# Kernel tuning notes

Hardware: AMD Instinct MI355X
Metric: run time of the kernel (lower is better)

Reference implementation:

```python
import jax, jax.numpy as jnp
import numpy as np
from jax import lax

D_MODEL = 64      # feature_dim
D_STATE = 16      # state_dim
D_CONV = 4        # conv_dim
EXPAND = 2
D_INNER = EXPAND * D_MODEL          # 128
DT_RANK = (D_MODEL + 15) // 16      # ceil(d_model/16) = 4, mamba default
IN_DIM = 64
LN_EPS = 1e-3                        # keras LayerNormalization default epsilon


def setup_inputs() -> dict:
    key = jax.random.key(0)
    ks = jax.random.split(key, 12)
    B, L = 16, 8192
    s = 0.02
    x = jax.random.normal(ks[0], (B, L, IN_DIM), jnp.float32)
    W_in = jax.random.normal(ks[1], (IN_DIM, D_MODEL), jnp.float32) * s
    b_in = jnp.zeros((D_MODEL,), jnp.float32)
    in_proj_w = jax.random.normal(ks[2], (D_MODEL, 2 * D_INNER), jnp.float32) * s
    conv_w = jax.random.normal(ks[3], (D_INNER, D_CONV), jnp.float32) * 0.1
    conv_b = jnp.zeros((D_INNER,), jnp.float32)
    x_proj_w = jax.random.normal(ks[4], (D_INNER, DT_RANK + 2 * D_STATE), jnp.float32) * s
    dt_proj_w = jax.random.normal(ks[5], (DT_RANK, D_INNER), jnp.float32) * (DT_RANK ** -0.5)
    # dt bias init so softplus(dt) lands roughly in [dt_min, dt_max]
    dt = jnp.exp(jax.random.uniform(ks[6], (D_INNER,)) * (np.log(0.1) - np.log(0.001)) + np.log(0.001))
    dt_proj_b = dt + jnp.log(-jnp.expm1(-dt))  # inverse softplus
    A_log = jnp.log(jnp.broadcast_to(jnp.arange(1, D_STATE + 1, dtype=jnp.float32), (D_INNER, D_STATE)))
    D_skip = jnp.ones((D_INNER,), jnp.float32)
    out_proj_w = jax.random.normal(ks[7], (D_INNER, D_MODEL), jnp.float32) * s
    ln_gamma = jnp.ones((D_MODEL,), jnp.float32)
    ln_beta = jnp.zeros((D_MODEL,), jnp.float32)
    return {"x": x, "W_in": W_in, "b_in": b_in, "in_proj_w": in_proj_w,
            "conv_w": conv_w, "conv_b": conv_b, "x_proj_w": x_proj_w,
            "dt_proj_w": dt_proj_w, "dt_proj_b": dt_proj_b, "A_log": A_log,
            "D_skip": D_skip, "out_proj_w": out_proj_w,
            "ln_gamma": ln_gamma, "ln_beta": ln_beta}


def reference(x, W_in, b_in, in_proj_w, conv_w, conv_b, x_proj_w,
              dt_proj_w, dt_proj_b, A_log, D_skip, out_proj_w, ln_gamma, ln_beta):
    B, L, _ = x.shape
    # Conv1D kernel_size=1 input projection
    xin = x @ W_in + b_in                          # [B,L,D_MODEL]
    # --- Mamba ---
    xz = xin @ in_proj_w                           # [B,L,2*D_INNER]
    xc, z = xz[..., :D_INNER], xz[..., D_INNER:]
    # causal depthwise conv (groups=d_inner, padding=d_conv-1, crop to L)
    xp = jnp.pad(xc, ((0, 0), (D_CONV - 1, 0), (0, 0)))
    xconv = conv_b
    for k in range(D_CONV):
        xconv = xconv + xp[:, k:k + L, :] * conv_w[:, k]
    u = jax.nn.silu(xconv)                         # [B,L,D_INNER]
    dbc = u @ x_proj_w                             # [B,L,DT_RANK+2*D_STATE]
    dt = jax.nn.softplus(dbc[..., :DT_RANK] @ dt_proj_w + dt_proj_b)   # [B,L,D_INNER]
    Bm = dbc[..., DT_RANK:DT_RANK + D_STATE]       # [B,L,D_STATE]
    Cm = dbc[..., DT_RANK + D_STATE:]              # [B,L,D_STATE]
    A = -jnp.exp(A_log)                            # [D_INNER,D_STATE]

    def step(h, xs):
        dt_t, b_t, c_t, u_t = xs                   # [B,Di],[B,Ds],[B,Ds],[B,Di]
        dA = jnp.exp(dt_t[:, :, None] * A)         # [B,Di,Ds]
        h = dA * h + (dt_t * u_t)[:, :, None] * b_t[:, None, :]
        y = jnp.einsum('bds,bs->bd', h, c_t)
        return h, y

    xs = (jnp.swapaxes(dt, 0, 1), jnp.swapaxes(Bm, 0, 1),
          jnp.swapaxes(Cm, 0, 1), jnp.swapaxes(u, 0, 1))
    h0 = jnp.zeros((B, D_INNER, D_STATE), x.dtype)
    _, ys = lax.scan(step, h0, xs)                 # ys: [L,B,D_INNER]
    y = jnp.swapaxes(ys, 0, 1) + u * D_skip
    y = y * jax.nn.silu(z)
    h_out = y @ out_proj_w                         # [B,L,D_MODEL]
    # residual + LayerNorm
    res = h_out + xin
    mu = jnp.mean(res, axis=-1, keepdims=True)
    var = jnp.mean(jnp.square(res - mu), axis=-1, keepdims=True)
    return ln_gamma * (res - mu) * lax.rsqrt(var + LN_EPS) + ln_beta
```

## Files before the change

### kernel.cpp

```cpp
#include <hip/hip_runtime.h>
#include <hip/hip_bf16.h>

#define B_SZ   16
#define L_SZ   8192
#define DM     64
#define DI     128
#define NCH    128
#define CLEN   64
#define CH     64
#define RT     80
#define PA     72
#define PU     136
#define PC     132
#define LN_EPS 1e-3f

typedef float  f4 __attribute__((ext_vector_type(4)));
typedef short  s8 __attribute__((ext_vector_type(8)));
typedef unsigned short u16;
typedef unsigned int   u32;
#define MFMA16 __builtin_amdgcn_mfma_f32_16x16x32_bf16

__device__ __forceinline__ u16 f2bfu(float f) {
    u32 u = __float_as_uint(f);
    return (u16)((u + 0x7FFFu + ((u >> 16) & 1u)) >> 16);
}
__device__ __forceinline__ u32 pk2bf(float a, float b) {
    return (u32)f2bfu(a) | ((u32)f2bfu(b) << 16);
}
__device__ __forceinline__ float bflo(u32 u) { return __uint_as_float(u << 16); }
__device__ __forceinline__ float bfhi(u32 u) { return __uint_as_float(u & 0xFFFF0000u); }
__device__ __forceinline__ float bfu2f(u16 h) { return __uint_as_float((u32)h << 16); }
__device__ __forceinline__ float fsig(float v) {
    return __builtin_amdgcn_rcpf(1.f + __expf(-v));
}
__device__ __forceinline__ float fsp(float v) {
    return fmaxf(v, 0.f) + __logf(1.f + __expf(-fabsf(v)));
}

__global__ __launch_bounds__(256) void k_prep(
    const float* __restrict__ W_in, const float* __restrict__ in_proj,
    const float* __restrict__ x_proj, const float* __restrict__ Wout,
    u16* __restrict__ Wf1, u16* __restrict__ Wf2,
    u16* __restrict__ Wf3, u16* __restrict__ Wf4)
{
    const int tid = threadIdx.x;
    for (int g = tid; g < 512; g += 256) {
        int lane = g & 63, ks = (g >> 6) & 1, nt = g >> 7;
        int n = nt * 16 + (lane & 15), kb = ks * 32 + (lane >> 4) * 8;
        for (int j = 0; j < 8; j++) Wf1[g * 8 + j] = f2bfu(W_in[(kb + j) * 64 + n]);
    }
    for (int g = tid; g < 2048; g += 256) {
        int lane = g & 63, ks = (g >> 6) & 1, nt = g >> 7;
        int n = nt * 16 + (lane & 15), kb = ks * 32 + (lane >> 4) * 8;
        for (int j = 0; j < 8; j++) Wf2[g * 8 + j] = f2bfu(in_proj[(kb + j) * 256 + n]);
    }
    for (int g = tid; g < 768; g += 256) {
        int lane = g & 63, ks = (g >> 6) & 3, nt = g >> 8;
        int n = nt * 16 + (lane & 15), kb = ks * 32 + (lane >> 4) * 8;
        for (int j = 0; j < 8; j++)
            Wf3[g * 8 + j] = f2bfu(n < 36 ? x_proj[(kb + j) * 36 + n] : 0.f);
    }
    for (int g = tid; g < 1024; g += 256) {
        int lane = g & 63, ks = (g >> 6) & 3, nt = g >> 8;
        int n = nt * 16 + (lane & 15), kb = ks * 32 + (lane >> 4) * 8;
        for (int j = 0; j < 8; j++) Wf4[g * 8 + j] = f2bfu(Wout[(kb + j) * 64 + n]);
    }
}

__global__ __launch_bounds__(256) void k_frontend(
    const float* __restrict__ x, const float* __restrict__ b_in,
    const float* __restrict__ conv_w, const float* __restrict__ conv_b,
    const float* __restrict__ dt_w, const float* __restrict__ dt_b,
    const u16* __restrict__ Wf1, const u16* __restrict__ Wf2, const u16* __restrict__ Wf3,
    float* __restrict__ xin_g, u16* __restrict__ u_g, float* __restrict__ dt_g,
    float* __restrict__ B_g, float* __restrict__ C_g, u16* __restrict__ sz_g)
{
    __shared__ __align__(16) char sm[41088];
    u16*   smA   = (u16*)sm;
    u16*   smB   = (u16*)(sm + 11520);
    u16*   smU   = (u16*)sm;
    float* smDtr = (float*)(sm + 17408);
    u16*   smC   = (u16*)(sm + 23040);

    const int tid = threadIdx.x;
    const int w = tid >> 6, lane = tid & 63;
    const int n16 = lane & 15, quad = lane >> 4;
    const int b = blockIdx.y, c0 = blockIdx.x * CH;
    const long long tokbase = (long long)b * L_SZ + c0;

    for (int idx = tid; idx < RT * 16; idx += 256) {
        int r = idx >> 4, c4 = idx & 15;
        int l = c0 - 3 + r;
        float4 v = make_float4(0.f, 0.f, 0.f, 0.f);
        if (r < 67 && l >= 0)
            v = *(const float4*)(x + ((long long)b * L_SZ + l) * 64 + c4 * 4);
        *(uint2*)((char*)smA + r * 144 + c4 * 8) = make_uint2(pk2bf(v.x, v.y), pk2bf(v.z, v.w));
    }
    __syncthreads();

    {
        s8 b0 = *(const s8*)(Wf1 + ((w * 2 + 0) * 64 + lane) * 8);
        s8 b1 = *(const s8*)(Wf1 + ((w * 2 + 1) * 64 + lane) * 8);
        float bias = b_in[w * 16 + n16];
        for (int m = 0; m < 5; m++) {
            int ar = m * 16 + n16;
            s8 a0 = *(const s8*)(smA + ar * PA + quad * 8);
            s8 a1 = *(const s8*)(smA + ar * PA + 32 + quad * 8);
            f4 acc = {0.f, 0.f, 0.f, 0.f};
            acc = MFMA16(a0, b0, acc, 0, 0, 0);
            acc = MFMA16(a1, b1, acc, 0, 0, 0);
#pragma unroll
            for (int reg = 0; reg < 4; reg++) {
                int rr = m * 16 + quad * 4 + reg;
                float v = acc[reg] + bias;
                smB[rr * PA + w * 16 + n16] = f2bfu(v);
                if (rr >= 3 && rr < 67)
                    xin_g[(tokbase + rr - 3) * 64 + w * 16 + n16] = v;
            }
        }
    }
    __syncthreads();

    {
        s8 bf[4][2];
#pragma unroll
        for (int i = 0; i < 4; i++)
#pragma unroll
            for (int ks = 0; ks < 2; ks++)
                bf[i][ks] = *(const s8*)(Wf2 + (((w * 4 + i) * 2 + ks) * 64 + lane) * 8);
        for (int m = 0; m < 5; m++) {
            int ar = m * 16 + n16;
            s8 a0 = *(const s8*)(smB + ar * PA + quad * 8);
            s8 a1 = *(const s8*)(smB + ar * PA + 32 + quad * 8);
#pragma unroll
            for (int i = 0; i < 4; i++) {
                f4 acc = {0.f, 0.f, 0.f, 0.f};
                acc = MFMA16(a0, bf[i][0], acc, 0, 0, 0);
                acc = MFMA16(a1, bf[i][1], acc, 0, 0, 0);
                int cg = (w * 4 + i) * 16 + n16;
#pragma unroll
                for (int reg = 0; reg < 4; reg++) {
                    int rr = m * 16 + quad * 4 + reg;
                    float v = acc[reg];
                    if (cg < 128) {
                        if (rr < 67) {
                            int l = c0 - 3 + rr;
                            smC[rr * PC + cg] = f2bfu(l >= 0 ? v : 0.f);
                        }
                    } else if (rr >= 3 && rr < 67) {
                        sz_g[(tokbase + rr - 3) * 128 + (cg - 128)] = f2bfu(v * fsig(v));
                    }
                }
            }
        }
    }
    __syncthreads();

    {
        const int d2 = lane * 2, ctb = w * 16;
        float4 cw0 = ((const float4*)conv_w)[d2];
        float4 cw1 = ((const float4*)conv_w)[d2 + 1];
        float cb0 = conv_b[d2], cb1 = conv_b[d2 + 1];
        u32 r0 = *(const u32*)((char*)smC + (ctb + 0) * 264 + lane * 4);
        u32 r1 = *(const u32*)((char*)smC + (ctb + 1) * 264 + lane * 4);
        u32 r2 = *(const u32*)((char*)smC + (ctb + 2) * 264 + lane * 4);
#pragma unroll 4
        for (int j = 0; j < 16; j++) {
            int ct = ctb + j;
            u32 r3 = *(const u32*)((char*)smC + (ct + 3) * 264 + lane * 4);
            float v0 = cb0 + bflo(r0) * cw0.x + bflo(r1) * cw0.y + bflo(r2) * cw0.z + bflo(r3) * cw0.w;
            float v1 = cb1 + bfhi(r0) * cw1.x + bfhi(r1) * cw1.y + bfhi(r2) * cw1.z + bfhi(r3) * cw1.w;
            u32 pk = pk2bf(v0 * fsig(v0), v1 * fsig(v1));
            *(u32*)(u_g + (tokbase + ct) * 128 + d2) = pk;
            *(u32*)(smU + ct * PU + d2) = pk;
            r0 = r1; r1 = r2; r2 = r3;
        }
    }
    __syncthreads();

    {
        s8 bf3[3][4];
#pragma unroll
        for (int nt = 0; nt < 3; nt++)
#pragma unroll
            for (int ks = 0; ks < 4; ks++)
                bf3[nt][ks] = *(const s8*)(Wf3 + ((nt * 4 + ks) * 64 + lane) * 8);
        f4 acc[3] = {{0.f,0.f,0.f,0.f},{0.f,0.f,0.f,0.f},{0.f,0.f,0.f,0.f}};
        int ar = w * 16 + n16;
#pragma unroll
        for (int ks = 0; ks < 4; ks++) {
            s8 a = *(const s8*)(smU + ar * PU + ks * 32 + quad * 8);
#pragma unroll
            for (int nt = 0; nt < 3; nt++) acc[nt] = MFMA16(a, bf3[nt][ks], acc[nt], 0, 0, 0);
        }
#pragma unroll
        for (int nt = 0; nt < 3; nt++) {
            int c = nt * 16 + n16;
#pragma unroll
            for (int reg = 0; reg < 4; reg++) {
                int rr = w * 16 + quad * 4 + reg;
                float v = acc[nt][reg];
                long long t = tokbase + rr;
                if (c < 4)       smDtr[rr * 4 + c] = v;
                else if (c < 20) B_g[t * 16 + (c - 4)] = v;
                else if (c < 36) C_g[t * 16 + (c - 20)] = v;
            }
        }
    }
    __syncthreads();

    {
        const int o2 = lane * 2, grp = w;
        float w00 = dt_w[o2],       w01 = dt_w[o2 + 1];
        float w10 = dt_w[128 + o2], w11 = dt_w[128 + o2 + 1];
        float w20 = dt_w[256 + o2], w21 = dt_w[256 + o2 + 1];
        float w30 = dt_w[384 + o2], w31 = dt_w[384 + o2 + 1];
        float b0 = dt_b[o2], b1 = dt_b[o2 + 1];
#pragma unroll 4
        for (int j = 0; j < 16; j++) {
            int ct = grp * 16 + j;
            float4 q = *(const float4*)(smDtr + ct * 4);
            float v0 = b0 + q.x * w00 + q.y * w10 + q.z * w20 + q.w * w30;
            float v1 = b1 + q.x * w01 + q.y * w11 + q.z * w21 + q.w * w31;
            *(float2*)(dt_g + (tokbase + ct) * 128 + o2) = make_float2(fsp(v0), fsp(v1));
        }
    }
}

__global__ __launch_bounds__(128) void k_scan1(
    const float* __restrict__ dt_g, const u16* __restrict__ u_g,
    const float* __restrict__ B_g, const float* __restrict__ A_log,
    float* __restrict__ hl_ws, float* __restrict__ sdt_ws)
{
    const int d = threadIdx.x, c = blockIdx.x, b = blockIdx.y;
    float A[16];
#pragma unroll
    for (int s = 0; s < 16; s++) A[s] = -__expf(A_log[d * 16 + s]);
    const float A0 = A[0];
    bool chain = true;
#pragma unroll
    for (int s = 1; s < 16; s++)
        chain = chain && (fabsf(A[s] - (float)(s + 1) * A0) <= 1e-4f * fabsf(A[s]));

    float h[16];
#pragma unroll
    for (int s = 0; s < 16; s++) h[s] = 0.f;
    float sdt = 0.f;
    const long long tok0 = (long long)b * L_SZ + (long long)c * CLEN;

    if (chain) {
        for (int i = 0; i < CLEN; i++) {
            const long long t = tok0 + i;
            float dtv = dt_g[t * 128 + d];
            float uv  = bfu2f(u_g[t * 128 + d]);
            const float4* Bp = (const float4*)(B_g + t * 16);
            float4 B0 = Bp[0], B1 = Bp[1], B2 = Bp[2], B3 = Bp[3];
            float Bv[16] = { B0.x, B0.y, B0.z, B0.w, B1.x, B1.y, B1.z, B1.w,
                             B2.x, B2.y, B2.z, B2.w, B3.x, B3.y, B3.z, B3.w };
            float du = dtv * uv;  sdt += dtv;
            float p = __expf(dtv * A0), dA = p;
            h[0] = dA * h[0] + du * Bv[0];
#pragma unroll
            for (int s = 1; s < 16; s++) { dA *= p; h[s] = dA * h[s] + du * Bv[s]; }
        }
    } else {
        for (int i = 0; i < CLEN; i++) {
            const long long t = tok0 + i;
            float dtv = dt_g[t * 128 + d];
            float uv  = bfu2f(u_g[t * 128 + d]);
            const float4* Bp = (const float4*)(B_g + t * 16);
            float4 B0 = Bp[0], B1 = Bp[1], B2 = Bp[2], B3 = Bp[3];
            float Bv[16] = { B0.x, B0.y, B0.z, B0.w, B1.x, B1.y, B1.z, B1.w,
                             B2.x, B2.y, B2.z, B2.w, B3.x, B3.y, B3.z, B3.w };
            float du = dtv * uv;  sdt += dtv;
#pragma unroll
            for (int s = 0; s < 16; s++) h[s] = __expf(dtv * A[s]) * h[s] + du * Bv[s];
        }
    }

    float4* hp4 = (float4*)(hl_ws + (((long long)b * NCH + c) * 128 + d) * 16);
    hp4[0] = make_float4(h[0], h[1], h[2], h[3]);
    hp4[1] = make_float4(h[4], h[5], h[6], h[7]);
    hp4[2] = make_float4(h[8], h[9], h[10], h[11]);
    hp4[3] = make_float4(h[12], h[13], h[14], h[15]);
    sdt_ws[((long long)b * NCH + c) * 128 + d] = sdt;
}

__global__ __launch_bounds__(256) void k_combine(
    const float* __restrict__ A_log, const float* __restrict__ hl_ws,
    const float* __restrict__ sdt_ws, float* __restrict__ hin_ws)
{
    int gid = blockIdx.x * 256 + threadIdx.x;
    int b = gid >> 11;
    int rem = gid & 2047;
    int d = rem >> 4;
    float A = -__expf(A_log[rem]);
    float h = 0.f;
    for (int c = 0; c < NCH; c++) {
        long long o = ((long long)b * NCH + c) * 2048 + rem;
        hin_ws[o] = h;
        float sdt = sdt_ws[((long long)b * NCH + c) * 128 + d];
        h = __expf(A * sdt) * h + hl_ws[o];
    }
}

__global__ __launch_bounds__(128) void k_scan3(
    const float* __restrict__ dt_g, const u16* __restrict__ u_g,
    const float* __restrict__ B_g, const float* __restrict__ C_g,
    const u16* __restrict__ sz_g, const float* __restrict__ A_log,
    const float* __restrict__ D_skip, const float* __restrict__ hin_ws,
    u16* __restrict__ y_g)
{
    const int d = threadIdx.x, c = blockIdx.x, b = blockIdx.y;
    float A[16];
#pragma unroll
    for (int s = 0; s < 16; s++) A[s] = -__expf(A_log[d * 16 + s]);
    const float A0 = A[0];
    bool chain = true;
#pragma unroll
    for (int s = 1; s < 16; s++)
        chain = chain && (fabsf(A[s] - (float)(s + 1) * A0) <= 1e-4f * fabsf(A[s]));

    float h[16];
    {
        const float4* hp = (const float4*)(hin_ws + (((long long)b * NCH + c) * 128 + d) * 16);
        float4 h0 = hp[0], h1 = hp[1], h2 = hp[2], h3 = hp[3];
        h[0]=h0.x; h[1]=h0.y; h[2]=h0.z; h[3]=h0.w;
        h[4]=h1.x; h[5]=h1.y; h[6]=h1.z; h[7]=h1.w;
        h[8]=h2.x; h[9]=h2.y; h[10]=h2.z; h[11]=h2.w;
        h[12]=h3.x; h[13]=h3.y; h[14]=h3.z; h[15]=h3.w;
    }
    const float Dv = D_skip[d];
    const long long tok0 = (long long)b * L_SZ + (long long)c * CLEN;

    if (chain) {
        for (int i = 0; i < CLEN; i++) {
            const long long t = tok0 + i;
            float dtv = dt_g[t * 128 + d];
            float uv  = bfu2f(u_g[t * 128 + d]);
            const float4* Bp = (const float4*)(B_g + t * 16);
            float4 B0 = Bp[0], B1 = Bp[1], B2 = Bp[2], B3 = Bp[3];
            float Bv[16] = { B0.x, B0.y, B0.z, B0.w, B1.x, B1.y, B1.z, B1.w,
                             B2.x, B2.y, B2.z, B2.w, B3.x, B3.y, B3.z, B3.w };
            const float4* Cp = (const float4*)(C_g + t * 16);
            float4 C0 = Cp[0], C1 = Cp[1], C2 = Cp[2], C3 = Cp[3];
            float Cv[16] = { C0.x, C0.y, C0.z, C0.w, C1.x, C1.y, C1.z, C1.w,
                             C2.x, C2.y, C2.z, C2.w, C3.x, C3.y, C3.z, C3.w };
            float du = dtv * uv;
            float p = __expf(dtv * A0), dA = p;
            h[0] = dA * h[0] + du * Bv[0];
            float ysum = h[0] * Cv[0];
#pragma unroll
            for (int s = 1; s < 16; s++) {
                dA *= p;
                h[s] = dA * h[s] + du * Bv[s];
                ysum += h[s] * Cv[s];
            }
            float szv = bfu2f(sz_g[t * 128 + d]);
            y_g[t * 128 + d] = f2bfu((ysum + uv * Dv) * szv);
        }
    } else {
        for (int i = 0; i < CLEN; i++) {
            const long long t = tok0 + i;
            float dtv = dt_g[t * 128 + d];
            float uv  = bfu2f(u_g[t * 128 + d]);
            const float4* Bp = (const float4*)(B_g + t * 16);
            float4 B0 = Bp[0], B1 = Bp[1], B2 = Bp[2], B3 = Bp[3];
            float Bv[16] = { B0.x, B0.y, B0.z, B0.w, B1.x, B1.y, B1.z, B1.w,
                             B2.x, B2.y, B2.z, B2.w, B3.x, B3.y, B3.z, B3.w };
            const float4* Cp = (const float4*)(C_g + t * 16);
            float4 C0 = Cp[0], C1 = Cp[1], C2 = Cp[2], C3 = Cp[3];
            float Cv[16] = { C0.x, C0.y, C0.z, C0.w, C1.x, C1.y, C1.z, C1.w,
                             C2.x, C2.y, C2.z, C2.w, C3.x, C3.y, C3.z, C3.w };
            float du = dtv * uv;
            float ysum = 0.f;
#pragma unroll
            for (int s = 0; s < 16; s++) {
                h[s] = __expf(dtv * A[s]) * h[s] + du * Bv[s];
                ysum += h[s] * Cv[s];
            }
            float szv = bfu2f(sz_g[t * 128 + d]);
            y_g[t * 128 + d] = f2bfu((ysum + uv * Dv) * szv);
        }
    }
}

__global__ __launch_bounds__(256) void k_epilogue(
    const u16* __restrict__ y_g, const float* __restrict__ xin_g,
    const u16* __restrict__ Wf4, const float* __restrict__ gamma,
    const float* __restrict__ beta, float* __restrict__ out)
{
    __shared__ __align__(16) char sm[34048];
    u16*   yA  = (u16*)sm;
    float* smR = (float*)(sm + 17408);

    const int tid = threadIdx.x;
    const int w = tid >> 6, lane = tid & 63;
    const int n16 = lane & 15, quad = lane >> 4;
    const long long t0 = (long long)blockIdx.x * 64;

    for (int idx = tid; idx < 64 * 64; idx += 256) {
        int r = idx >> 6, cp = idx & 63;
        u32 v = ((const u32*)y_g)[(t0 + r) * 64 + cp];
        *(u32*)((char*)yA + r * 272 + cp * 4) = v;
    }
    __syncthreads();

    {
        s8 bf[4];
#pragma unroll
        for (int ks = 0; ks < 4; ks++)
            bf[ks] = *(const s8*)(Wf4 + ((w * 4 + ks) * 64 + lane) * 8);
#pragma unroll
        for (int m = 0; m < 4; m++) {
            int ar = m * 16 + n16;
            f4 acc = {0.f, 0.f, 0.f, 0.f};
#pragma unroll
            for (int ks = 0; ks < 4; ks++) {
                s8 a = *(const s8*)(yA + ar * PU + ks * 32 + quad * 8);
                acc = MFMA16(a, bf[ks], acc, 0, 0, 0);
            }
#pragma unroll
            for (int reg = 0; reg < 4; reg++) {
                int rr = m * 16 + quad * 4 + reg;
                smR[rr * 65 + w * 16 + n16] = acc[reg];
            }
        }
    }
    __syncthreads();

    {
        int o = tid & 63, wv = tid >> 6;
        float g = gamma[o], bb = beta[o];
        for (int j = 0; j < 16; j++) {
            int rr = wv * 16 + j;
            float r = smR[rr * 65 + o] + xin_g[(t0 + rr) * 64 + o];
            float s = r;
#pragma unroll
            for (int mS = 0; mS < 6; mS++) s += __shfl_xor(s, 1 << mS, 64);
            float mu = s * (1.f / 64.f);
            float dv = r - mu;
            float vs = dv * dv;
#pragma unroll
            for (int mS = 0; mS < 6; mS++) vs += __shfl_xor(vs, 1 << mS, 64);
            out[(t0 + rr) * 64 + o] = g * dv * rsqrtf(vs * (1.f / 64.f) + LN_EPS) + bb;
        }
    }
}

extern "C" void kernel_launch(void* const* d_in, const int* in_sizes, int n_in,
                              void* d_out, int out_size, void* d_ws, size_t ws_size,
                              hipStream_t stream)
{
    const float* x       = (const float*)d_in[0];
    const float* W_in    = (const float*)d_in[1];
    const float* b_in    = (const float*)d_in[2];
    const float* in_proj = (const float*)d_in[3];
    const float* conv_w  = (const float*)d_in[4];
    const float* conv_b  = (const float*)d_in[5];
    const float* x_proj  = (const float*)d_in[6];
    const float* dt_w    = (const float*)d_in[7];
    const float* dt_b    = (const float*)d_in[8];
    const float* A_log   = (const float*)d_in[9];
    const float* D_skip  = (const float*)d_in[10];
    const float* Wout    = (const float*)d_in[11];
    const float* gamma   = (const float*)d_in[12];
    const float* beta    = (const float*)d_in[13];
    float* out = (float*)d_out;

    const long long NT = (long long)B_SZ * L_SZ;
    char* ws = (char*)d_ws;
    float*  xin_g = (float*)ws;   ws += NT * 64 * 4;
    float*  dt_g  = (float*)ws;   ws += NT * 128 * 4;
    float*  B_g   = (float*)ws;   ws += NT * 16 * 4;
    float*  C_g   = (float*)ws;   ws += NT * 16 * 4;
    u16*    u_g   = (u16*)ws;     ws += NT * 128 * 2;
    u16*    sz_g  = (u16*)ws;     ws += NT * 128 * 2;
    u16*    y_g   = (u16*)ws;     ws += NT * 128 * 2;
    float*  hl_ws  = (float*)ws;  ws += (long long)B_SZ * NCH * 2048 * 4;
    float*  sdt_ws = (float*)ws;  ws += (long long)B_SZ * NCH * 128 * 4;
    float*  hin_ws = (float*)ws;  ws += (long long)B_SZ * NCH * 2048 * 4;
    u16* Wf1 = (u16*)ws; ws += 4096 * 2;
    u16* Wf2 = (u16*)ws; ws += 16384 * 2;
    u16* Wf3 = (u16*)ws; ws += 6144 * 2;
    u16* Wf4 = (u16*)ws; ws += 8192 * 2;

    k_prep<<<1, 256, 0, stream>>>(W_in, in_proj, x_proj, Wout, Wf1, Wf2, Wf3, Wf4);

    k_frontend<<<dim3(L_SZ / CH, B_SZ), 256, 0, stream>>>(
        x, b_in, conv_w, conv_b, dt_w, dt_b, Wf1, Wf2, Wf3,
        xin_g, u_g, dt_g, B_g, C_g, sz_g);

    k_scan1<<<dim3(NCH, B_SZ), 128, 0, stream>>>(
        dt_g, u_g, B_g, A_log, hl_ws, sdt_ws);

    k_combine<<<128, 256, 0, stream>>>(A_log, hl_ws, sdt_ws, hin_ws);

    k_scan3<<<dim3(NCH, B_SZ), 128, 0, stream>>>(
        dt_g, u_g, B_g, C_g, sz_g, A_log, D_skip, hin_ws, y_g);

    k_epilogue<<<2048, 256, 0, stream>>>(y_g, xin_g, Wf4, gamma, beta, out);
}
```

Baseline: 311.6 us.

## Split scan state across thread pairs and pack fp16 dt with bf16 u

The scan kernels now use two threads per channel, each owning 8 of the 16 state entries, so each block has twice as many threads. The partial outputs are combined with a lane shuffle. dt is stored as fp16 and packed with bf16 u into one 32-bit word, so the scans read one stream instead of two and the separate u write from the frontend is dropped. The B and dt loads for the next token are issued one step ahead of use. The cost is lower precision for dt, duplicated B/C/dt loads across the thread pair, and a shuffle per token.

```diff
diff --git a/kernel.cpp b/kernel.cpp
--- a/kernel.cpp
+++ b/kernel.cpp
@@ -1,5 +1,6 @@
 #include <hip/hip_runtime.h>
 #include <hip/hip_bf16.h>
+#include <hip/hip_fp16.h>
 
 #define B_SZ   16
 #define L_SZ   8192
@@ -30,6 +31,9 @@
 __device__ __forceinline__ float bflo(u32 u) { return __uint_as_float(u << 16); }
 __device__ __forceinline__ float bfhi(u32 u) { return __uint_as_float(u & 0xFFFF0000u); }
 __device__ __forceinline__ float bfu2f(u16 h) { return __uint_as_float((u32)h << 16); }
+__device__ __forceinline__ float h2f(u32 lo16) {
+    return __half2float(__ushort_as_half((u16)(lo16 & 0xFFFFu)));
+}
 __device__ __forceinline__ float fsig(float v) {
     return __builtin_amdgcn_rcpf(1.f + __expf(-v));
 }
@@ -72,7 +76,7 @@
     const float* __restrict__ conv_w, const float* __restrict__ conv_b,
     const float* __restrict__ dt_w, const float* __restrict__ dt_b,
     const u16* __restrict__ Wf1, const u16* __restrict__ Wf2, const u16* __restrict__ Wf3,
-    float* __restrict__ xin_g, u16* __restrict__ u_g, float* __restrict__ dt_g,
+    float* __restrict__ xin_g, u32* __restrict__ dtu_g,
     float* __restrict__ B_g, float* __restrict__ C_g, u16* __restrict__ sz_g)
 {
     __shared__ __align__(16) char sm[41088];
@@ -171,7 +175,6 @@
             float v0 = cb0 + bflo(r0) * cw0.x + bflo(r1) * cw0.y + bflo(r2) * cw0.z + bflo(r3) * cw0.w;
             float v1 = cb1 + bfhi(r0) * cw1.x + bfhi(r1) * cw1.y + bfhi(r2) * cw1.z + bfhi(r3) * cw1.w;
             u32 pk = pk2bf(v0 * fsig(v0), v1 * fsig(v1));
-            *(u32*)(u_g + (tokbase + ct) * 128 + d2) = pk;
             *(u32*)(smU + ct * PU + d2) = pk;
             r0 = r1; r1 = r2; r2 = r3;
         }
@@ -222,68 +225,90 @@
             float4 q = *(const float4*)(smDtr + ct * 4);
             float v0 = b0 + q.x * w00 + q.y * w10 + q.z * w20 + q.w * w30;
             float v1 = b1 + q.x * w01 + q.y * w11 + q.z * w21 + q.w * w31;
-            *(float2*)(dt_g + (tokbase + ct) * 128 + o2) = make_float2(fsp(v0), fsp(v1));
-        }
-    }
-}
-
-__global__ __launch_bounds__(128) void k_scan1(
-    const float* __restrict__ dt_g, const u16* __restrict__ u_g,
-    const float* __restrict__ B_g, const float* __restrict__ A_log,
+            u32 upk = *(const u32*)(smU + ct * PU + o2);
+            u32 pk0 = (u32)__half_as_ushort(__float2half_rn(fsp(v0))) | (upk << 16);
+            u32 pk1 = (u32)__half_as_ushort(__float2half_rn(fsp(v1))) | (upk & 0xFFFF0000u);
+            *(uint2*)(dtu_g + (tokbase + ct) * 128 + o2) = make_uint2(pk0, pk1);
+        }
+    }
+}
+
+__global__ __launch_bounds__(256, 8) void k_scan1(
+    const u32* __restrict__ dtu_g, const float* __restrict__ B_g,
+    const float* __restrict__ A_log,
     float* __restrict__ hl_ws, float* __restrict__ sdt_ws)
 {
-    const int d = threadIdx.x, c = blockIdx.x, b = blockIdx.y;
-    float A[16];
-#pragma unroll
-    for (int s = 0; s < 16; s++) A[s] = -__expf(A_log[d * 16 + s]);
-    const float A0 = A[0];
-    bool chain = true;
-#pragma unroll
-    for (int s = 1; s < 16; s++)
-        chain = chain && (fabsf(A[s] - (float)(s + 1) * A0) <= 1e-4f * fabsf(A[s]));
-
-    float h[16];
-#pragma unroll
-    for (int s = 0; s < 16; s++) h[s] = 0.f;
+    const int tid = threadIdx.x;
+    const int d = tid >> 1, sh = tid & 1, s0 = sh * 8;
+    const int c = blockIdx.x, b = blockIdx.y;
+    const float A0g = -__expf(A_log[d * 16]);
+    float A[8];
+#pragma unroll
+    for (int s = 0; s < 8; s++) A[s] = -__expf(A_log[d * 16 + s0 + s]);
+    bool chl = true;
+#pragma unroll
+    for (int s = 0; s < 8; s++)
+        chl = chl && (fabsf(A[s] - (float)(s0 + s + 1) * A0g) <= 1e-4f * fabsf(A[s]));
+    const bool chain = __all(chl);
+
+    float h[8];
+#pragma unroll
+    for (int s = 0; s < 8; s++) h[s] = 0.f;
     float sdt = 0.f;
     const long long tok0 = (long long)b * L_SZ + (long long)c * CLEN;
 
+    u32 pk = dtu_g[tok0 * 128 + d];
+    float4 Bq0 = *(const float4*)(B_g + tok0 * 16 + s0);
+    float4 Bq1 = *(const float4*)(B_g + tok0 * 16 + s0 + 4);
+
     if (chain) {
+#pragma unroll 2
         for (int i = 0; i < CLEN; i++) {
             const long long t = tok0 + i;
-            float dtv = dt_g[t * 128 + d];
-            float uv  = bfu2f(u_g[t * 128 + d]);
-            const float4* Bp = (const float4*)(B_g + t * 16);
-            float4 B0 = Bp[0], B1 = Bp[1], B2 = Bp[2], B3 = Bp[3];
-            float Bv[16] = { B0.x, B0.y, B0.z, B0.w, B1.x, B1.y, B1.z, B1.w,
-                             B2.x, B2.y, B2.z, B2.w, B3.x, B3.y, B3.z, B3.w };
-            float du = dtv * uv;  sdt += dtv;
-            float p = __expf(dtv * A0), dA = p;
-            h[0] = dA * h[0] + du * Bv[0];
-#pragma unroll
-            for (int s = 1; s < 16; s++) { dA *= p; h[s] = dA * h[s] + du * Bv[s]; }
+            u32 pkc = pk; float4 b0 = Bq0, b1 = Bq1;
+            if (i + 1 < CLEN) {
+                pk  = dtu_g[(t + 1) * 128 + d];
+                Bq0 = *(const float4*)(B_g + (t + 1) * 16 + s0);
+                Bq1 = *(const float4*)(B_g + (t + 1) * 16 + s0 + 4);
+            }
+            float dtv = h2f(pkc);
+            float uv  = bfhi(pkc);
+            float du  = dtv * uv;  sdt += dtv;
+            float p  = __expf(dtv * A0g);
+            float p2 = p * p, p4 = p2 * p2;
+            float dA = sh ? p4 * p4 * p : p;
+            h[0] = dA * h[0] + du * b0.x;
+            dA *= p; h[1] = dA * h[1] + du * b0.y;
+            dA *= p; h[2] = dA * h[2] + du * b0.z;
+            dA *= p; h[3] = dA * h[3] + du * b0.w;
+            dA *= p; h[4] = dA * h[4] + du * b1.x;
+            dA *= p; h[5] = dA * h[5] + du * b1.y;
+            dA *= p; h[6] = dA * h[6] + du * b1.z;
+            dA *= p; h[7] = dA * h[7] + du * b1.w;
         }
     } else {
+#pragma unroll 2
         for (int i = 0; i < CLEN; i++) {
             const long long t = tok0 + i;
-            float dtv = dt_g[t * 128 + d];
-            float uv  = bfu2f(u_g[t * 128 + d]);
-            const float4* Bp = (const float4*)(B_g + t * 16);
-            float4 B0 = Bp[0], B1 = Bp[1], B2 = Bp[2], B3 = Bp[3];
-            float Bv[16] = { B0.x, B0.y, B0.z, B0.w, B1.x, B1.y, B1.z, B1.w,
-                             B2.x, B2.y, B2.z, B2.w, B3.x, B3.y, B3.z, B3.w };
-            float du = dtv * uv;  sdt += dtv;
-#pragma unroll
-            for (int s = 0; s < 16; s++) h[s] = __expf(dtv * A[s]) * h[s] + du * Bv[s];
-        }
-    }
-
-    float4* hp4 = (float4*)(hl_ws + (((long long)b * NCH + c) * 128 + d) * 16);
+            u32 pkc = pk; float4 b0 = Bq0, b1 = Bq1;
+            if (i + 1 < CLEN) {
+                pk  = dtu_g[(t + 1) * 128 + d];
+                Bq0 = *(const float4*)(B_g + (t + 1) * 16 + s0);
+                Bq1 = *(const float4*)(B_g + (t + 1) * 16 + s0 + 4);
+            }
+            float dtv = h2f(pkc);
+            float uv  = bfhi(pkc);
+            float du  = dtv * uv;  sdt += dtv;
+            float Bv[8] = { b0.x, b0.y, b0.z, b0.w, b1.x, b1.y, b1.z, b1.w };
+#pragma unroll
+            for (int s = 0; s < 8; s++) h[s] = __expf(dtv * A[s]) * h[s] + du * Bv[s];
+        }
+    }
+
+    float4* hp4 = (float4*)(hl_ws + (((long long)b * NCH + c) * 128 + d) * 16 + s0);
     hp4[0] = make_float4(h[0], h[1], h[2], h[3]);
     hp4[1] = make_float4(h[4], h[5], h[6], h[7]);
-    hp4[2] = make_float4(h[8], h[9], h[10], h[11]);
-    hp4[3] = make_float4(h[12], h[13], h[14], h[15]);
-    sdt_ws[((long long)b * NCH + c) * 128 + d] = sdt;
+    if (sh == 0) sdt_ws[((long long)b * NCH + c) * 128 + d] = sdt;
 }
 
 __global__ __launch_bounds__(256) void k_combine(
@@ -304,83 +329,97 @@
     }
 }
 
-__global__ __launch_bounds__(128) void k_scan3(
-    const float* __restrict__ dt_g, const u16* __restrict__ u_g,
-    const float* __restrict__ B_g, const float* __restrict__ C_g,
-    const u16* __restrict__ sz_g, const float* __restrict__ A_log,
-    const float* __restrict__ D_skip, const float* __restrict__ hin_ws,
-    u16* __restrict__ y_g)
-{
-    const int d = threadIdx.x, c = blockIdx.x, b = blockIdx.y;
-    float A[16];
-#pragma unroll
-    for (int s = 0; s < 16; s++) A[s] = -__expf(A_log[d * 16 + s]);
-    const float A0 = A[0];
-    bool chain = true;
-#pragma unroll
-    for (int s = 1; s < 16; s++)
-        chain = chain && (fabsf(A[s] - (float)(s + 1) * A0) <= 1e-4f * fabsf(A[s]));
-
-    float h[16];
-    {
-        const float4* hp = (const float4*)(hin_ws + (((long long)b * NCH + c) * 128 + d) * 16);
-        float4 h0 = hp[0], h1 = hp[1], h2 = hp[2], h3 = hp[3];
+__global__ __launch_bounds__(256, 8) void k_scan3(
+    const u32* __restrict__ dtu_g, const float* __restrict__ B_g,
+    const float* __restrict__ C_g, const u16* __restrict__ sz_g,
+    const float* __restrict__ A_log, const float* __restrict__ D_skip,
+    const float* __restrict__ hin_ws, u16* __restrict__ y_g)
+{
+    const int tid = threadIdx.x;
+    const int d = tid >> 1, sh = tid & 1, s0 = sh * 8;
+    const int c = blockIdx.x, b = blockIdx.y;
+    const float A0g = -__expf(A_log[d * 16]);
+    float A[8];
+#pragma unroll
+    for (int s = 0; s < 8; s++) A[s] = -__expf(A_log[d * 16 + s0 + s]);
+    bool chl = true;
+#pragma unroll
+    for (int s = 0; s < 8; s++)
+        chl = chl && (fabsf(A[s] - (float)(s0 + s + 1) * A0g) <= 1e-4f * fabsf(A[s]));
+    const bool chain = __all(chl);
+
+    float h[8];
+    {
+        const float4* hp = (const float4*)(hin_ws + (((long long)b * NCH + c) * 128 + d) * 16 + s0);
+        float4 h0 = hp[0], h1 = hp[1];
         h[0]=h0.x; h[1]=h0.y; h[2]=h0.z; h[3]=h0.w;
         h[4]=h1.x; h[5]=h1.y; h[6]=h1.z; h[7]=h1.w;
-        h[8]=h2.x; h[9]=h2.y; h[10]=h2.z; h[11]=h2.w;
-        h[12]=h3.x; h[13]=h3.y; h[14]=h3.z; h[15]=h3.w;
     }
     const float Dv = D_skip[d];
     const long long tok0 = (long long)b * L_SZ + (long long)c * CLEN;
 
+    u32 pk = dtu_g[tok0 * 128 + d];
+    float4 Bq0 = *(const float4*)(B_g + tok0 * 16 + s0);
+    float4 Bq1 = *(const float4*)(B_g + tok0 * 16 + s0 + 4);
+
     if (chain) {
+#pragma unroll 2
         for (int i = 0; i < CLEN; i++) {
             const long long t = tok0 + i;
-            float dtv = dt_g[t * 128 + d];
-            float uv  = bfu2f(u_g[t * 128 + d]);
-            const float4* Bp = (const float4*)(B_g + t * 16);
-            float4 B0 = Bp[0], B1 = Bp[1], B2 = Bp[2], B3 = Bp[3];
-            float Bv[16] = { B0.x, B0.y, B0.z, B0.w, B1.x, B1.y, B1.z, B1.w,
-                             B2.x, B2.y, B2.z, B2.w, B3.x, B3.y, B3.z, B3.w };
-            const float4* Cp = (const float4*)(C_g + t * 16);
-            float4 C0 = Cp[0], C1 = Cp[1], C2 = Cp[2], C3 = Cp[3];
-            float Cv[16] = { C0.x, C0.y, C0.z, C0.w, C1.x, C1.y, C1.z, C1.w,
-                             C2.x, C2.y, C2.z, C2.w, C3.x, C3.y, C3.z, C3.w };
-            float du = dtv * uv;
-            float p = __expf(dtv * A0), dA = p;
-            h[0] = dA * h[0] + du * Bv[0];
-            float ysum = h[0] * Cv[0];
-#pragma unroll
-            for (int s = 1; s < 16; s++) {
-                dA *= p;
-                h[s] = dA * h[s] + du * Bv[s];
-                ysum += h[s] * Cv[s];
-            }
-            float szv = bfu2f(sz_g[t * 128 + d]);
-            y_g[t * 128 + d] = f2bfu((ysum + uv * Dv) * szv);
+            u32 pkc = pk; float4 b0 = Bq0, b1 = Bq1;
+            float4 c0 = *(const float4*)(C_g + t * 16 + s0);
+            float4 c1 = *(const float4*)(C_g + t * 16 + s0 + 4);
+            u16 szu = sz_g[t * 128 + d];
+            if (i + 1 < CLEN) {
+                pk  = dtu_g[(t + 1) * 128 + d];
+                Bq0 = *(const float4*)(B_g + (t + 1) * 16 + s0);
+                Bq1 = *(const float4*)(B_g + (t + 1) * 16 + s0 + 4);
+            }
+            float dtv = h2f(pkc);
+            float uv  = bfhi(pkc);
+            float du  = dtv * uv;
+            float p  = __expf(dtv * A0g);
+            float p2 = p * p, p4 = p2 * p2;
+            float dA = sh ? p4 * p4 * p : p;
+            h[0] = dA * h[0] + du * b0.x; float ys = h[0] * c0.x;
+            dA *= p; h[1] = dA * h[1] + du * b0.y; ys += h[1] * c0.y;
+            dA *= p; h[2] = dA * h[2] + du * b0.z; ys += h[2] * c0.z;
+            dA *= p; h[3] = dA * h[3] + du * b0.w; ys += h[3] * c0.w;
+            dA *= p; h[4] = dA * h[4] + du * b1.x; ys += h[4] * c1.x;
+            dA *= p; h[5] = dA * h[5] + du * b1.y; ys += h[5] * c1.y;
+            dA *= p; h[6] = dA * h[6] + du * b1.z; ys += h[6] * c1.z;
+            dA *= p; h[7] = dA * h[7] + du * b1.w; ys += h[7] * c1.w;
+            ys += __shfl_xor(ys, 1, 64);
+            if (sh == 0)
+                y_g[t * 128 + d] = f2bfu((ys + uv * Dv) * bfu2f(szu));
         }
     } else {
+#pragma unroll 2
         for (int i = 0; i < CLEN; i++) {
             const long long t = tok0 + i;
-            float dtv = dt_g[t * 128 + d];
-            float uv  = bfu2f(u_g[t * 128 + d]);
-            const float4* Bp = (const float4*)(B_g + t * 16);
-            float4 B0 = Bp[0], B1 = Bp[1], B2 = Bp[2], B3 = Bp[3];
-            float Bv[16] = { B0.x, B0.y, B0.z, B0.w, B1.x, B1.y, B1.z, B1.w,
-                             B2.x, B2.y, B2.z, B2.w, B3.x, B3.y, B3.z, B3.w };
-            const float4* Cp = (const float4*)(C_g + t * 16);
-            float4 C0 = Cp[0], C1 = Cp[1], C2 = Cp[2], C3 = Cp[3];
-            float Cv[16] = { C0.x, C0.y, C0.z, C0.w, C1.x, C1.y, C1.z, C1.w,
-                             C2.x, C2.y, C2.z, C2.w, C3.x, C3.y, C3.z, C3.w };
-            float du = dtv * uv;
-            float ysum = 0.f;
-#pragma unroll
-            for (int s = 0; s < 16; s++) {
+            u32 pkc = pk; float4 b0 = Bq0, b1 = Bq1;
+            float4 c0 = *(const float4*)(C_g + t * 16 + s0);
+            float4 c1 = *(const float4*)(C_g + t * 16 + s0 + 4);
+            u16 szu = sz_g[t * 128 + d];
+            if (i + 1 < CLEN) {
+                pk  = dtu_g[(t + 1) * 128 + d];
+                Bq0 = *(const float4*)(B_g + (t + 1) * 16 + s0);
+                Bq1 = *(const float4*)(B_g + (t + 1) * 16 + s0 + 4);
+            }
+            float dtv = h2f(pkc);
+            float uv  = bfhi(pkc);
+            float du  = dtv * uv;
+            float Bv[8] = { b0.x, b0.y, b0.z, b0.w, b1.x, b1.y, b1.z, b1.w };
+            float Cv[8] = { c0.x, c0.y, c0.z, c0.w, c1.x, c1.y, c1.z, c1.w };
+            float ys = 0.f;
+#pragma unroll
+            for (int s = 0; s < 8; s++) {
                 h[s] = __expf(dtv * A[s]) * h[s] + du * Bv[s];
-                ysum += h[s] * Cv[s];
-            }
-            float szv = bfu2f(sz_g[t * 128 + d]);
-            y_g[t * 128 + d] = f2bfu((ysum + uv * Dv) * szv);
+                ys += h[s] * Cv[s];
+            }
+            ys += __shfl_xor(ys, 1, 64);
+            if (sh == 0)
+                y_g[t * 128 + d] = f2bfu((ys + uv * Dv) * bfu2f(szu));
         }
     }
 }
@@ -471,10 +510,9 @@
     const long long NT = (long long)B_SZ * L_SZ;
     char* ws = (char*)d_ws;
     float*  xin_g = (float*)ws;   ws += NT * 64 * 4;
-    float*  dt_g  = (float*)ws;   ws += NT * 128 * 4;
+    u32*    dtu_g = (u32*)ws;     ws += NT * 128 * 4;
     float*  B_g   = (float*)ws;   ws += NT * 16 * 4;
     float*  C_g   = (float*)ws;   ws += NT * 16 * 4;
-    u16*    u_g   = (u16*)ws;     ws += NT * 128 * 2;
     u16*    sz_g  = (u16*)ws;     ws += NT * 128 * 2;
     u16*    y_g   = (u16*)ws;     ws += NT * 128 * 2;
     float*  hl_ws  = (float*)ws;  ws += (long long)B_SZ * NCH * 2048 * 4;
@@ -489,15 +527,15 @@
 
     k_frontend<<<dim3(L_SZ / CH, B_SZ), 256, 0, stream>>>(
         x, b_in, conv_w, conv_b, dt_w, dt_b, Wf1, Wf2, Wf3,
-        xin_g, u_g, dt_g, B_g, C_g, sz_g);
-
-    k_scan1<<<dim3(NCH, B_SZ), 128, 0, stream>>>(
-        dt_g, u_g, B_g, A_log, hl_ws, sdt_ws);
+        xin_g, dtu_g, B_g, C_g, sz_g);
+
+    k_scan1<<<dim3(NCH, B_SZ), 256, 0, stream>>>(
+        dtu_g, B_g, A_log, hl_ws, sdt_ws);
 
     k_combine<<<128, 256, 0, stream>>>(A_log, hl_ws, sdt_ws, hin_ws);
 
-    k_scan3<<<dim3(NCH, B_SZ), 128, 0, stream>>>(
-        dt_g, u_g, B_g, C_g, sz_g, A_log, D_skip, hin_ws, y_g);
+    k_scan3<<<dim3(NCH, B_SZ), 256, 0, stream>>>(
+        dtu_g, B_g, C_g, sz_g, A_log, D_skip, hin_ws, y_g);
 
     k_epilogue<<<2048, 256, 0, stream>>>(y_g, xin_g, Wf4, gamma, beta, out);
 }
```

Result: slower. 366.9 us (+17.7%).

## Pack dt (fp16) and u (bf16) into one word and stage chunks in LDS

Applied to the files above, without the earlier changes.

The frontend now writes dt as fp16 and u as bf16 packed into a single 32-bit word per channel, in place of a separate fp32 dt array and a bf16 u array. This cuts dt+u traffic from 6 to 4 bytes per element. Both scan kernels first copy their 64-token chunk of packed dt/u into shared memory with wide vector loads, then read from LDS inside the sequential loop. The fp16 rounding of dt adds a precision loss, and the 32 KB LDS buffer per block may lower scan occupancy.

```diff
diff --git a/kernel.cpp b/kernel.cpp
--- a/kernel.cpp
+++ b/kernel.cpp
@@ -1,5 +1,6 @@
 #include <hip/hip_runtime.h>
 #include <hip/hip_bf16.h>
+#include <hip/hip_fp16.h>
 
 #define B_SZ   16
 #define L_SZ   8192
@@ -30,6 +31,9 @@
 __device__ __forceinline__ float bflo(u32 u) { return __uint_as_float(u << 16); }
 __device__ __forceinline__ float bfhi(u32 u) { return __uint_as_float(u & 0xFFFF0000u); }
 __device__ __forceinline__ float bfu2f(u16 h) { return __uint_as_float((u32)h << 16); }
+__device__ __forceinline__ float h2f(u32 lo16) {
+    return __half2float(__ushort_as_half((u16)(lo16 & 0xFFFFu)));
+}
 __device__ __forceinline__ float fsig(float v) {
     return __builtin_amdgcn_rcpf(1.f + __expf(-v));
 }
@@ -72,7 +76,7 @@
     const float* __restrict__ conv_w, const float* __restrict__ conv_b,
     const float* __restrict__ dt_w, const float* __restrict__ dt_b,
     const u16* __restrict__ Wf1, const u16* __restrict__ Wf2, const u16* __restrict__ Wf3,
-    float* __restrict__ xin_g, u16* __restrict__ u_g, float* __restrict__ dt_g,
+    float* __restrict__ xin_g, u32* __restrict__ dtu_g,
     float* __restrict__ B_g, float* __restrict__ C_g, u16* __restrict__ sz_g)
 {
     __shared__ __align__(16) char sm[41088];
@@ -171,7 +175,6 @@
             float v0 = cb0 + bflo(r0) * cw0.x + bflo(r1) * cw0.y + bflo(r2) * cw0.z + bflo(r3) * cw0.w;
             float v1 = cb1 + bfhi(r0) * cw1.x + bfhi(r1) * cw1.y + bfhi(r2) * cw1.z + bfhi(r3) * cw1.w;
             u32 pk = pk2bf(v0 * fsig(v0), v1 * fsig(v1));
-            *(u32*)(u_g + (tokbase + ct) * 128 + d2) = pk;
             *(u32*)(smU + ct * PU + d2) = pk;
             r0 = r1; r1 = r2; r2 = r3;
         }
@@ -222,17 +225,30 @@
             float4 q = *(const float4*)(smDtr + ct * 4);
             float v0 = b0 + q.x * w00 + q.y * w10 + q.z * w20 + q.w * w30;
             float v1 = b1 + q.x * w01 + q.y * w11 + q.z * w21 + q.w * w31;
-            *(float2*)(dt_g + (tokbase + ct) * 128 + o2) = make_float2(fsp(v0), fsp(v1));
+            u32 upk = *(const u32*)(smU + ct * PU + o2);
+            u32 pk0 = (u32)__half_as_ushort(__float2half_rn(fsp(v0))) | (upk << 16);
+            u32 pk1 = (u32)__half_as_ushort(__float2half_rn(fsp(v1))) | (upk & 0xFFFF0000u);
+            *(uint2*)(dtu_g + (tokbase + ct) * 128 + o2) = make_uint2(pk0, pk1);
         }
     }
 }
 
 __global__ __launch_bounds__(128) void k_scan1(
-    const float* __restrict__ dt_g, const u16* __restrict__ u_g,
-    const float* __restrict__ B_g, const float* __restrict__ A_log,
+    const u32* __restrict__ dtu_g, const float* __restrict__ B_g,
+    const float* __restrict__ A_log,
     float* __restrict__ hl_ws, float* __restrict__ sdt_ws)
 {
+    __shared__ __align__(16) u32 sdtu[CLEN * 128];
     const int d = threadIdx.x, c = blockIdx.x, b = blockIdx.y;
+    const long long tok0 = (long long)b * L_SZ + (long long)c * CLEN;
+
+    {
+        const uint4* src = (const uint4*)(dtu_g + tok0 * 128);
+        uint4* dst = (uint4*)sdtu;
+#pragma unroll
+        for (int k = 0; k < 16; k++) dst[d + k * 128] = src[d + k * 128];
+    }
+
     float A[16];
 #pragma unroll
     for (int s = 0; s < 16; s++) A[s] = -__expf(A_log[d * 16 + s]);
@@ -246,14 +262,14 @@
 #pragma unroll
     for (int s = 0; s < 16; s++) h[s] = 0.f;
     float sdt = 0.f;
-    const long long tok0 = (long long)b * L_SZ + (long long)c * CLEN;
+    __syncthreads();
 
     if (chain) {
         for (int i = 0; i < CLEN; i++) {
-            const long long t = tok0 + i;
-            float dtv = dt_g[t * 128 + d];
-            float uv  = bfu2f(u_g[t * 128 + d]);
-            const float4* Bp = (const float4*)(B_g + t * 16);
+            u32 pk = sdtu[i * 128 + d];
+            float dtv = h2f(pk);
+            float uv  = bfhi(pk);
+            const float4* Bp = (const float4*)(B_g + (tok0 + i) * 16);
             float4 B0 = Bp[0], B1 = Bp[1], B2 = Bp[2], B3 = Bp[3];
             float Bv[16] = { B0.x, B0.y, B0.z, B0.w, B1.x, B1.y, B1.z, B1.w,
                              B2.x, B2.y, B2.z, B2.w, B3.x, B3.y, B3.z, B3.w };
@@ -265,10 +281,10 @@
         }
     } else {
         for (int i = 0; i < CLEN; i++) {
-            const long long t = tok0 + i;
-            float dtv = dt_g[t * 128 + d];
-            float uv  = bfu2f(u_g[t * 128 + d]);
-            const float4* Bp = (const float4*)(B_g + t * 16);
+            u32 pk = sdtu[i * 128 + d];
+            float dtv = h2f(pk);
+            float uv  = bfhi(pk);
+            const float4* Bp = (const float4*)(B_g + (tok0 + i) * 16);
             float4 B0 = Bp[0], B1 = Bp[1], B2 = Bp[2], B3 = Bp[3];
             float Bv[16] = { B0.x, B0.y, B0.z, B0.w, B1.x, B1.y, B1.z, B1.w,
                              B2.x, B2.y, B2.z, B2.w, B3.x, B3.y, B3.z, B3.w };
@@ -305,13 +321,22 @@
 }
 
 __global__ __launch_bounds__(128) void k_scan3(
-    const float* __restrict__ dt_g, const u16* __restrict__ u_g,
-    const float* __restrict__ B_g, const float* __restrict__ C_g,
-    const u16* __restrict__ sz_g, const float* __restrict__ A_log,
-    const float* __restrict__ D_skip, const float* __restrict__ hin_ws,
-    u16* __restrict__ y_g)
-{
+    const u32* __restrict__ dtu_g, const float* __restrict__ B_g,
+    const float* __restrict__ C_g, const u16* __restrict__ sz_g,
+    const float* __restrict__ A_log, const float* __restrict__ D_skip,
+    const float* __restrict__ hin_ws, u16* __restrict__ y_g)
+{
+    __shared__ __align__(16) u32 sdtu[CLEN * 128];
     const int d = threadIdx.x, c = blockIdx.x, b = blockIdx.y;
+    const long long tok0 = (long long)b * L_SZ + (long long)c * CLEN;
+
+    {
+        const uint4* src = (const uint4*)(dtu_g + tok0 * 128);
+        uint4* dst = (uint4*)sdtu;
+#pragma unroll
+        for (int k = 0; k < 16; k++) dst[d + k * 128] = src[d + k * 128];
+    }
+
     float A[16];
 #pragma unroll
     for (int s = 0; s < 16; s++) A[s] = -__expf(A_log[d * 16 + s]);
@@ -331,13 +356,14 @@
         h[12]=h3.x; h[13]=h3.y; h[14]=h3.z; h[15]=h3.w;
     }
     const float Dv = D_skip[d];
-    const long long tok0 = (long long)b * L_SZ + (long long)c * CLEN;
+    __syncthreads();
 
     if (chain) {
         for (int i = 0; i < CLEN; i++) {
             const long long t = tok0 + i;
-            float dtv = dt_g[t * 128 + d];
-            float uv  = bfu2f(u_g[t * 128 + d]);
+            u32 pk = sdtu[i * 128 + d];
+            float dtv = h2f(pk);
+            float uv  = bfhi(pk);
             const float4* Bp = (const float4*)(B_g + t * 16);
             float4 B0 = Bp[0], B1 = Bp[1], B2 = Bp[2], B3 = Bp[3];
             float Bv[16] = { B0.x, B0.y, B0.z, B0.w, B1.x, B1.y, B1.z, B1.w,
@@ -362,8 +388,9 @@
     } else {
         for (int i = 0; i < CLEN; i++) {
             const long long t = tok0 + i;
-            float dtv = dt_g[t * 128 + d];
-            float uv  = bfu2f(u_g[t * 128 + d]);
+            u32 pk = sdtu[i * 128 + d];
+            float dtv = h2f(pk);
+            float uv  = bfhi(pk);
             const float4* Bp = (const float4*)(B_g + t * 16);
             float4 B0 = Bp[0], B1 = Bp[1], B2 = Bp[2], B3 = Bp[3];
             float Bv[16] = { B0.x, B0.y, B0.z, B0.w, B1.x, B1.y, B1.z, B1.w,
@@ -471,10 +498,9 @@
     const long long NT = (long long)B_SZ * L_SZ;
     char* ws = (char*)d_ws;
     float*  xin_g = (float*)ws;   ws += NT * 64 * 4;
-    float*  dt_g  = (float*)ws;   ws += NT * 128 * 4;
+    u32*    dtu_g = (u32*)ws;     ws += NT * 128 * 4;
     float*  B_g   = (float*)ws;   ws += NT * 16 * 4;
     float*  C_g   = (float*)ws;   ws += NT * 16 * 4;
-    u16*    u_g   = (u16*)ws;     ws += NT * 128 * 2;
     u16*    sz_g  = (u16*)ws;     ws += NT * 128 * 2;
     u16*    y_g   = (u16*)ws;     ws += NT * 128 * 2;
     float*  hl_ws  = (float*)ws;  ws += (long long)B_SZ * NCH * 2048 * 4;
@@ -489,15 +515,15 @@
 
     k_frontend<<<dim3(L_SZ / CH, B_SZ), 256, 0, stream>>>(
         x, b_in, conv_w, conv_b, dt_w, dt_b, Wf1, Wf2, Wf3,
-        xin_g, u_g, dt_g, B_g, C_g, sz_g);
+        xin_g, dtu_g, B_g, C_g, sz_g);
 
     k_scan1<<<dim3(NCH, B_SZ), 128, 0, stream>>>(
-        dt_g, u_g, B_g, A_log, hl_ws, sdt_ws);
+        dtu_g, B_g, A_log, hl_ws, sdt_ws);
 
     k_combine<<<128, 256, 0, stream>>>(A_log, hl_ws, sdt_ws, hin_ws);
 
     k_scan3<<<dim3(NCH, B_SZ), 128, 0, stream>>>(
-        dt_g, u_g, B_g, C_g, sz_g, A_log, D_skip, hin_ws, y_g);
+        dtu_g, B_g, C_g, sz_g, A_log, D_skip, hin_ws, y_g);
 
     k_epilogue<<<2048, 256, 0, stream>>>(y_g, xin_g, Wf4, gamma, beta, out);
 }
```

Result: slower. 363.3 us (+16.6%).
